# Kernel tuning notes

Measured on AMD Instinct MI355X. Metric: run time of the kernel, lower is better.

## Reference

```python
import jax, jax.numpy as jnp
import numpy as np

N_HEAD, N_MIX, D_MODEL, D_K, D_V = 8, 2, 512, 64, 64
BN_EPS = 1e-5


def avg_pool_3x3_s2(x):
    # AvgPool2d(kernel=3, stride=2, pad=1, count_include_pad=False) on NCHW
    win = (1, 1, 3, 3)
    stride = (1, 1, 2, 2)
    pad = [(0, 0), (0, 0), (1, 1), (1, 1)]
    s = jax.lax.reduce_window(x, 0.0, jax.lax.add, win, stride, pad)
    ones = jnp.ones((1, 1, x.shape[2], x.shape[3]), x.dtype)
    cnt = jax.lax.reduce_window(ones, 0.0, jax.lax.add, win, stride, pad)
    return s / cnt


def conv1x1(x, w, b=None):
    # w: [out_c, in_c]; x: [B, in_c, H, W]
    y = jnp.einsum('oc,bchw->bohw', w, x)
    if b is not None:
        y = y + b[None, :, None, None]
    return y


def setup_inputs() -> dict:
    key = jax.random.key(0)
    ks = jax.random.split(key, 8)
    B, H, W = 2, 56, 56
    std_kq = np.sqrt(2.0 / (D_MODEL + D_K)).astype(np.float32)
    std_v = np.sqrt(2.0 / (D_MODEL + D_V)).astype(np.float32)
    std_mix = np.power(N_MIX, -0.5).astype(np.float32)
    return {
        'x': jax.random.normal(ks[0], (B, D_MODEL, H, W), jnp.float32),
        'w_qs': jax.random.normal(ks[1], (N_HEAD * D_K, D_MODEL), jnp.float32) * std_kq,
        'b_qs': jnp.zeros((N_HEAD * D_K,), jnp.float32),
        'w_vs': jax.random.normal(ks[2], (N_HEAD * D_V, D_MODEL), jnp.float32) * std_v,
        'b_vs': jnp.zeros((N_HEAD * D_V,), jnp.float32),
        'mix_w': jax.random.uniform(ks[3], (N_MIX, D_K), jnp.float32, -std_mix, std_mix),
        'w_out': jax.random.normal(ks[4], (D_MODEL, N_HEAD * D_V), jnp.float32) * 0.02,
        'bn_gamma': jnp.ones((D_MODEL,), jnp.float32),
        'bn_beta': jnp.zeros((D_MODEL,), jnp.float32),
    }


def reference(x, w_qs, b_qs, w_vs, b_vs, mix_w, w_out, bn_gamma, bn_beta):
    B, C, H, W = x.shape
    N = H * W
    m = N_MIX
    d = D_K // m  # per-mixture dim
    temperature = D_K ** 0.5

    px = avg_pool_3x3_s2(x)  # [B, C, H/2, W/2]
    N2 = px.shape[2] * px.shape[3]

    # conv_ks aliases conv_qs in the original (shared weights)
    qt = conv1x1(x, w_qs, b_qs).reshape(B * N_HEAD, D_K, N)
    kt = conv1x1(px, w_qs, b_qs).reshape(B * N_HEAD, D_K, N2)
    vt = conv1x1(px, w_vs, b_vs).reshape(B * N_HEAD, D_V, N2)

    # mixture weights pi: softmax over mixtures of weight @ mean_q
    bar_qt = qt.mean(axis=2)  # [B', D_K]
    pi = jax.nn.softmax(jnp.einsum('md,bd->bm', mix_w, bar_qt), axis=1)  # [B', m]

    q = qt.reshape(B * N_HEAD * m, d, N).transpose(0, 2, 1)  # [B'm, N, d]
    k2 = kt.reshape(B * N_HEAD * m, d, N2)  # [B'm, d, N2]

    attn = jnp.einsum('bnd,bdk->bnk', q, k2) / temperature  # [B'm, N, N2]
    attn = jax.nn.softmax(attn, axis=2)
    # dropout is identity in eval mode
    attn = (attn * pi.reshape(-1, 1, 1)).reshape(B * N_HEAD, m, N, N2).sum(1)

    out = jnp.einsum('bnk,bvk->bnv', attn, vt)  # [B', N, D_V]
    out = out.transpose(0, 2, 1).reshape(B, N_HEAD * D_V, H, W)
    out = conv1x1(out, w_out)  # no bias
    # BatchNorm2d in eval mode: running_mean=0, running_var=1
    inv = 1.0 / jnp.sqrt(jnp.float32(1.0 + BN_EPS))
    out = out * inv * bn_gamma[None, :, None, None] + bn_beta[None, :, None, None]
    return out + x
```

## Files before the change

kernel.cpp:

```cpp
#include <hip/hip_runtime.h>
#include <math.h>

typedef unsigned short u16;
typedef short bf16x8 __attribute__((ext_vector_type(8)));
typedef short bf16x4 __attribute__((ext_vector_type(4)));
typedef float f32x4 __attribute__((ext_vector_type(4)));

#define MFMA(a, b, c) __builtin_amdgcn_mfma_f32_16x16x32_bf16(a, b, c, 0, 0, 0)

#define SCALE_K 0.18033688011112043f

__device__ __forceinline__ float bf2f(u16 v) {
    union { float f; unsigned u; } x;
    x.u = ((unsigned)v) << 16;
    return x.f;
}
__device__ __forceinline__ u16 f2bf(float f) {
    union { float f; unsigned u; } x;
    x.f = f;
    unsigned r = x.u + 0x7FFF + ((x.u >> 16) & 1);
    return (u16)(r >> 16);
}
__device__ __forceinline__ bf16x4 pk4(float a, float b, float c, float d) {
    union { unsigned u[2]; bf16x4 v; } x;
    asm("v_cvt_pk_bf16_f32 %0, %1, %2" : "=v"(x.u[0]) : "v"(a), "v"(b));
    asm("v_cvt_pk_bf16_f32 %0, %1, %2" : "=v"(x.u[1]) : "v"(c), "v"(d));
    return x.v;
}

__global__ __launch_bounds__(256) void cvt_kernel(const float* __restrict__ s0,
                                                  const float* __restrict__ s1,
                                                  const float* __restrict__ s2,
                                                  u16* __restrict__ d0, u16* __restrict__ d1,
                                                  u16* __restrict__ d2) {
    int i = blockIdx.x * 256 + threadIdx.x;
    const float* s = (blockIdx.y == 0) ? s0 : ((blockIdx.y == 1) ? s1 : s2);
    u16* d = (blockIdx.y == 0) ? d0 : ((blockIdx.y == 1) ? d1 : d2);
    d[i] = f2bf(s[i]);
}

__global__ __launch_bounds__(256) void transpose_kernel(const float* __restrict__ x,
                                                        u16* __restrict__ xT) {
    __shared__ u16 tile[64][65];
    int b = blockIdx.z;
    int n0 = blockIdx.x * 64, c0 = blockIdx.y * 64;
    int j = threadIdx.x & 63, q = threadIdx.x >> 6;
    const float* xb = x + b * 512 * 3136;
#pragma unroll
    for (int it = 0; it < 16; ++it) {
        int r = q * 16 + it;
        tile[r][j] = f2bf(xb[(c0 + r) * 3136 + n0 + j]);
    }
    __syncthreads();
    u16* xTb = xT + b * 3136 * 512;
#pragma unroll
    for (int it = 0; it < 16; ++it) {
        int r = q * 16 + it;
        xTb[(n0 + r) * 512 + c0 + j] = tile[j][r];
    }
}

__global__ __launch_bounds__(256) void pool_kernel(const u16* __restrict__ xT,
                                                   u16* __restrict__ pxT) {
    int n2 = blockIdx.x;
    int b = blockIdx.y;
    int t = threadIdx.x;
    int i = n2 / 28, jj = n2 % 28;
    float s0 = 0.f, s1 = 0.f;
    int cnt = 0;
    const u16* xb = xT + b * 3136 * 512;
#pragma unroll
    for (int dr = 0; dr < 3; dr++) {
        int r = 2 * i - 1 + dr;
        if (r < 0 || r >= 56) continue;
#pragma unroll
        for (int dc = 0; dc < 3; dc++) {
            int cc = 2 * jj - 1 + dc;
            if (cc < 0 || cc >= 56) continue;
            const u16* row = xb + (r * 56 + cc) * 512;
            s0 += bf2f(row[t]);
            s1 += bf2f(row[t + 256]);
            cnt++;
        }
    }
    float invc = 1.0f / (float)cnt;
    u16* op = pxT + (b * 784 + n2) * 512;
    op[t] = f2bf(s0 * invc);
    op[t + 256] = f2bf(s1 * invc);
}

__device__ __forceinline__ void gemm_core(const u16* __restrict__ A, int lda, int M,
                                          const u16* __restrict__ BT, int ldb, int Ncol,
                                          int K, int row0, int col0, f32x4 acc[4][4]) {
    int lane = threadIdx.x & 63;
    int lr = lane & 15, lg = lane >> 4;
    int ar[4], bc[4];
#pragma unroll
    for (int i = 0; i < 4; i++) {
        int r = row0 + i * 16 + lr;
        ar[i] = (r < M) ? r : (M - 1);
    }
#pragma unroll
    for (int j = 0; j < 4; j++) {
        int cj = col0 + j * 16 + lr;
        bc[j] = (cj < Ncol) ? cj : (Ncol - 1);
    }
    for (int k = 0; k < K; k += 32) {
        int ko = k + lg * 8;
        bf16x8 af[4], bfr[4];
#pragma unroll
        for (int i = 0; i < 4; i++) af[i] = *(const bf16x8*)(A + ar[i] * lda + ko);
#pragma unroll
        for (int j = 0; j < 4; j++) bfr[j] = *(const bf16x8*)(BT + bc[j] * ldb + ko);
#pragma unroll
        for (int i = 0; i < 4; i++)
#pragma unroll
            for (int j = 0; j < 4; j++) acc[i][j] = MFMA(af[i], bfr[j], acc[i][j]);
    }
}

__global__ __launch_bounds__(256) void gemm_qk(const u16* __restrict__ xT,
                                               const u16* __restrict__ W,
                                               const float* __restrict__ bias,
                                               u16* __restrict__ out, int M, int Npad,
                                               float oscale) {
    int b = blockIdx.z;
    int w = threadIdx.x >> 6;
    int row0 = blockIdx.y * 128 + (w >> 1) * 64;
    int col0 = blockIdx.x * 128 + (w & 1) * 64;
    f32x4 acc[4][4];
#pragma unroll
    for (int i = 0; i < 4; i++)
#pragma unroll
        for (int j = 0; j < 4; j++) acc[i][j] = (f32x4){0.f, 0.f, 0.f, 0.f};
    gemm_core(xT + b * M * 512, 512, M, W, 512, 512, 512, row0, col0, acc);
    int lane = threadIdx.x & 63;
    int lr = lane & 15, lg = lane >> 4;
#pragma unroll
    for (int j = 0; j < 4; j++) {
        int oc = col0 + j * 16 + lr;
        float bs = bias[oc];
        int bh = b * 8 + (oc >> 6), dk = oc & 63;
        u16* op = out + (bh * Npad) * 64 + dk;
#pragma unroll
        for (int i = 0; i < 4; i++) {
#pragma unroll
            for (int r = 0; r < 4; r++) {
                int n = row0 + i * 16 + lg * 4 + r;
                if (n < M) op[n * 64] = f2bf((acc[i][j][r] + bs) * oscale);
                else if (n < Npad) op[n * 64] = 0;
            }
        }
    }
}

__global__ __launch_bounds__(256) void gemm_v(const u16* __restrict__ W,
                                              const u16* __restrict__ pxT,
                                              const float* __restrict__ bias,
                                              u16* __restrict__ vt) {
    int b = blockIdx.z;
    int w = threadIdx.x >> 6;
    int row0 = blockIdx.y * 128 + (w >> 1) * 64;
    int col0 = blockIdx.x * 128 + (w & 1) * 64;
    f32x4 acc[4][4];
#pragma unroll
    for (int i = 0; i < 4; i++)
#pragma unroll
        for (int j = 0; j < 4; j++) acc[i][j] = (f32x4){0.f, 0.f, 0.f, 0.f};
    gemm_core(W, 512, 512, pxT + b * 784 * 512, 512, 784, 512, row0, col0, acc);
    int lane = threadIdx.x & 63;
    int lr = lane & 15, lg = lane >> 4;
#pragma unroll
    for (int i = 0; i < 4; i++) {
#pragma unroll
        for (int r = 0; r < 4; r++) {
            int oc = row0 + i * 16 + lg * 4 + r;
            float bs = bias[oc];
            u16* vp = vt + ((b * 8 + (oc >> 6)) * 64 + (oc & 63)) * 800;
#pragma unroll
            for (int j = 0; j < 4; j++) {
                int n2 = col0 + j * 16 + lr;
                if (n2 < 784) vp[n2] = f2bf(acc[i][j][r] + bs);
                else if (n2 < 800) vp[n2] = 0;
            }
        }
    }
}

__global__ __launch_bounds__(256) void pi_stage1(const u16* __restrict__ qt,
                                                 float* __restrict__ part) {
    __shared__ float red[4][64];
    int chunk = blockIdx.x, bh = blockIdx.y;
    int t = threadIdx.x, dk = t & 63, seg = t >> 6;
    const u16* q = qt + (bh * 3136 + chunk * 112) * 64 + dk;
    float s = 0.f;
    for (int n = seg; n < 112; n += 4) s += bf2f(q[n * 64]);
    red[seg][dk] = s;
    __syncthreads();
    if (t < 64) part[(bh * 28 + chunk) * 64 + t] =
        red[0][t] + red[1][t] + red[2][t] + red[3][t];
}

__global__ __launch_bounds__(64) void pi_stage2(const float* __restrict__ part,
                                                const float* __restrict__ mix_w,
                                                float* __restrict__ pi) {
    int bh = blockIdx.x, lane = threadIdx.x;
    float bar = 0.f;
#pragma unroll
    for (int c = 0; c < 28; c++) bar += part[(bh * 28 + c) * 64 + lane];
    bar *= (1.0f / 3136.0f);
    float l0 = mix_w[lane] * bar;
    float l1 = mix_w[64 + lane] * bar;
#pragma unroll
    for (int d = 1; d < 64; d <<= 1) {
        l0 += __shfl_xor(l0, d);
        l1 += __shfl_xor(l1, d);
    }
    if (lane == 0) {
        float mx = fmaxf(l0, l1);
        float e0 = __expf(l0 - mx), e1 = __expf(l1 - mx);
        float inv = 1.0f / (e0 + e1);
        pi[bh * 2 + 0] = e0 * inv;
        pi[bh * 2 + 1] = e1 * inv;
    }
}

__global__ __launch_bounds__(256) void attn_kernel(const u16* __restrict__ qt,
                                                   const u16* __restrict__ kt,
                                                   const u16* __restrict__ vt,
                                                   const float* __restrict__ pi,
                                                   u16* __restrict__ ao) {
    int w = threadIdx.x >> 6, lane = threadIdx.x & 63;
    int lr = lane & 15, lg = lane >> 4;
    int bh = blockIdx.x & 15;
    int xq = blockIdx.x >> 4;
    int qbase = (xq * 4 + w) * 16;
    const u16* qp = qt + (bh * 3136 + qbase) * 64;
    const u16* kp = kt + bh * 800 * 64;
    const u16* vp = vt + bh * 64 * 800;

    bf16x8 qf[2];
    qf[0] = *(const bf16x8*)(qp + lr * 64 + lg * 8);
    qf[1] = *(const bf16x8*)(qp + lr * 64 + 32 + lg * 8);

    f32x4 O[2][4];
    float lsum[2] = {0.f, 0.f};
#pragma unroll
    for (int m = 0; m < 2; m++)
#pragma unroll
        for (int t = 0; t < 4; t++) O[m][t] = (f32x4){0.f, 0.f, 0.f, 0.f};

    auto loadK = [&](int base, bf16x8 (*kf)[2]) {
#pragma unroll
        for (int m = 0; m < 2; m++) {
            kf[m][0] = *(const bf16x8*)(kp + (base + lr) * 64 + m * 32 + lg * 8);
            kf[m][1] = *(const bf16x8*)(kp + (base + 16 + lr) * 64 + m * 32 + lg * 8);
        }
    };
    auto loadV = [&](int base, bf16x4* v0, bf16x4* v1) {
#pragma unroll
        for (int t = 0; t < 4; t++) {
            v0[t] = *(const bf16x4*)(vp + (t * 16 + lr) * 800 + base + lg * 4);
            v1[t] = *(const bf16x4*)(vp + (t * 16 + lr) * 800 + base + 16 + lg * 4);
        }
    };
    auto compute = [&](bf16x8 (*kf)[2], bf16x4* v0, bf16x4* v1, bool tail) {
#pragma unroll
        for (int m = 0; m < 2; m++) {
            f32x4 s0 = MFMA(kf[m][0], qf[m], ((f32x4){0.f, 0.f, 0.f, 0.f}));
            f32x4 s1 = MFMA(kf[m][1], qf[m], ((f32x4){0.f, 0.f, 0.f, 0.f}));
            float p0 = __builtin_amdgcn_exp2f(s0[0]);
            float p1 = __builtin_amdgcn_exp2f(s0[1]);
            float p2 = __builtin_amdgcn_exp2f(s0[2]);
            float p3 = __builtin_amdgcn_exp2f(s0[3]);
            float p4 = __builtin_amdgcn_exp2f(s1[0]);
            float p5 = __builtin_amdgcn_exp2f(s1[1]);
            float p6 = __builtin_amdgcn_exp2f(s1[2]);
            float p7 = __builtin_amdgcn_exp2f(s1[3]);
            if (tail) { p4 = 0.f; p5 = 0.f; p6 = 0.f; p7 = 0.f; }
            lsum[m] += ((p0 + p1) + (p2 + p3)) + ((p4 + p5) + (p6 + p7));
            union { bf16x4 h[2]; bf16x8 w8; } pa;
            pa.h[0] = pk4(p0, p1, p2, p3);
            pa.h[1] = pk4(p4, p5, p6, p7);
#pragma unroll
            for (int t = 0; t < 4; t++) {
                union { bf16x4 h[2]; bf16x8 w8; } vv;
                vv.h[0] = v0[t];
                vv.h[1] = v1[t];
                O[m][t] = MFMA(pa.w8, vv.w8, O[m][t]);
            }
        }
    };

    bf16x8 kfA[2][2], kfB[2][2];
    bf16x4 v0A[4], v1A[4], v0B[4], v1B[4];
    loadK(0, kfA);
    loadV(0, v0A, v1A);
    for (int c = 0; c < 24; c += 2) {
        loadK((c + 1) * 32, kfB);
        loadV((c + 1) * 32, v0B, v1B);
        compute(kfA, v0A, v1A, false);
        loadK((c + 2) * 32, kfA);
        loadV((c + 2) * 32, v0A, v1A);
        compute(kfB, v0B, v1B, false);
    }
    compute(kfA, v0A, v1A, true);

#pragma unroll
    for (int m = 0; m < 2; m++) {
        lsum[m] += __shfl_xor(lsum[m], 16);
        lsum[m] += __shfl_xor(lsum[m], 32);
    }
    float pi0 = pi[bh * 2], pi1 = pi[bh * 2 + 1];
    int b = bh >> 3, h = bh & 7;
    u16* aop = ao + ((b * 3136 + qbase) * 512) + h * 64;
#pragma unroll
    for (int t = 0; t < 4; t++) {
#pragma unroll
        for (int r = 0; r < 4; r++) {
            int n = lg * 4 + r;
            float l0 = __shfl(lsum[0], n);
            float l1 = __shfl(lsum[1], n);
            float v = (pi0 / l0) * O[0][t][r] + (pi1 / l1) * O[1][t][r];
            aop[n * 512 + t * 16 + lr] = f2bf(v);
        }
    }
}

__global__ __launch_bounds__(256) void gemm_out(const u16* __restrict__ W,
                                                const u16* __restrict__ aoT,
                                                const float* __restrict__ gamma,
                                                const float* __restrict__ beta,
                                                const float* __restrict__ xres,
                                                float* __restrict__ out) {
    int b = blockIdx.z;
    int w = threadIdx.x >> 6;
    int row0 = blockIdx.y * 128 + (w >> 1) * 64;
    int col0 = blockIdx.x * 128 + (w & 1) * 64;
    f32x4 acc[4][4];
#pragma unroll
    for (int i = 0; i < 4; i++)
#pragma unroll
        for (int j = 0; j < 4; j++) acc[i][j] = (f32x4){0.f, 0.f, 0.f, 0.f};
    gemm_core(W, 512, 512, aoT + b * 3136 * 512, 512, 3136, 512, row0, col0, acc);
    const float inv = 0.99999500003749969f;
    int lane = threadIdx.x & 63;
    int lr = lane & 15, lg = lane >> 4;
#pragma unroll
    for (int i = 0; i < 4; i++) {
#pragma unroll
        for (int r = 0; r < 4; r++) {
            int oc = row0 + i * 16 + lg * 4 + r;
            float g = gamma[oc] * inv;
            float bt = beta[oc];
            const float* xp = xres + (b * 512 + oc) * 3136;
            float* op = out + (b * 512 + oc) * 3136;
#pragma unroll
            for (int j = 0; j < 4; j++) {
                int n = col0 + j * 16 + lr;
                if (n < 3136) op[n] = acc[i][j][r] * g + bt + xp[n];
            }
        }
    }
}

extern "C" void kernel_launch(void* const* d_in, const int* in_sizes, int n_in,
                              void* d_out, int out_size, void* d_ws, size_t ws_size,
                              hipStream_t stream) {
    const float* x = (const float*)d_in[0];
    const float* w_qs = (const float*)d_in[1];
    const float* b_qs = (const float*)d_in[2];
    const float* w_vs = (const float*)d_in[3];
    const float* b_vs = (const float*)d_in[4];
    const float* mix_w = (const float*)d_in[5];
    const float* w_out = (const float*)d_in[6];
    const float* gamma = (const float*)d_in[7];
    const float* beta = (const float*)d_in[8];
    float* out = (float*)d_out;

    char* ws = (char*)d_ws;
    u16* xT = (u16*)(ws + 0);
    u16* ao = (u16*)(ws + 0);
    u16* pxT = (u16*)(ws + 6422528);
    u16* qt = (u16*)(ws + 8028160);
    u16* kt = (u16*)(ws + 14450688);
    u16* vt = (u16*)(ws + 16089088);
    u16* wq_b = (u16*)(ws + 17727488);
    u16* wv_b = (u16*)(ws + 18251776);
    u16* wo_b = (u16*)(ws + 18776064);
    float* pi = (float*)(ws + 19300352);
    float* part = (float*)(ws + 19300480);

    hipLaunchKernelGGL(cvt_kernel, dim3(1024, 3), dim3(256), 0, stream, w_qs, w_vs, w_out,
                       wq_b, wv_b, wo_b);
    hipLaunchKernelGGL(transpose_kernel, dim3(49, 8, 2), dim3(256), 0, stream, x, xT);
    hipLaunchKernelGGL(pool_kernel, dim3(784, 2), dim3(256), 0, stream, xT, pxT);
    hipLaunchKernelGGL(gemm_qk, dim3(4, 25, 2), dim3(256), 0, stream, xT, wq_b, b_qs, qt,
                       3136, 3136, 1.0f);
    hipLaunchKernelGGL(gemm_qk, dim3(4, 7, 2), dim3(256), 0, stream, pxT, wq_b, b_qs, kt,
                       784, 800, SCALE_K);
    hipLaunchKernelGGL(gemm_v, dim3(7, 4, 2), dim3(256), 0, stream, wv_b, pxT, b_vs, vt);
    hipLaunchKernelGGL(pi_stage1, dim3(28, 16), dim3(256), 0, stream, qt, part);
    hipLaunchKernelGGL(pi_stage2, dim3(16), dim3(64), 0, stream, part, mix_w, pi);
    hipLaunchKernelGGL(attn_kernel, dim3(784), dim3(256), 0, stream, qt, kt, vt, pi, ao);
    hipLaunchKernelGGL(gemm_out, dim3(25, 4, 2), dim3(256), 0, stream, wo_b, ao, gamma,
                       beta, x, out);
}
```

Baseline: 242.7 us.

## Split attention KV range across waves with LDS reduction of partial outputs

Each block now handles a single 16-query tile, and its four waves each process a disjoint slice of the 25 key chunks, where previously each wave swept all keys for its own query tile. Partial output accumulators and row sums are written to shared memory and reduced across waves before normalisation and the bf16 store. The grid grows fourfold to expose more parallelism and shorten each wave's serial chain. In exchange it drops the explicit double-buffered prefetch, reloads Q per block, and adds LDS traffic and a barrier.

Result: faster. 229.1 us (-5.6%).

```diff
diff --git a/kernel.cpp b/kernel.cpp
--- a/kernel.cpp
+++ b/kernel.cpp
@@ -230,100 +230,119 @@
                                                    const u16* __restrict__ vt,
                                                    const float* __restrict__ pi,
                                                    u16* __restrict__ ao) {
+    __shared__ float ldsO[8][16][65];
+    __shared__ float ldsL[8][16];
     int w = threadIdx.x >> 6, lane = threadIdx.x & 63;
     int lr = lane & 15, lg = lane >> 4;
     int bh = blockIdx.x & 15;
-    int xq = blockIdx.x >> 4;
-    int qbase = (xq * 4 + w) * 16;
+    int qti = blockIdx.x >> 4;
+    int qbase = qti * 16;
     const u16* qp = qt + (bh * 3136 + qbase) * 64;
-    const u16* kp = kt + bh * 800 * 64;
-    const u16* vp = vt + bh * 64 * 800;
-
-    bf16x8 qf[2];
-    qf[0] = *(const bf16x8*)(qp + lr * 64 + lg * 8);
-    qf[1] = *(const bf16x8*)(qp + lr * 64 + 32 + lg * 8);
-
-    f32x4 O[2][4];
-    float lsum[2] = {0.f, 0.f};
-#pragma unroll
-    for (int m = 0; m < 2; m++)
-#pragma unroll
-        for (int t = 0; t < 4; t++) O[m][t] = (f32x4){0.f, 0.f, 0.f, 0.f};
-
-    auto loadK = [&](int base, bf16x8 (*kf)[2]) {
-#pragma unroll
-        for (int m = 0; m < 2; m++) {
-            kf[m][0] = *(const bf16x8*)(kp + (base + lr) * 64 + m * 32 + lg * 8);
-            kf[m][1] = *(const bf16x8*)(kp + (base + 16 + lr) * 64 + m * 32 + lg * 8);
-        }
-    };
-    auto loadV = [&](int base, bf16x4* v0, bf16x4* v1) {
-#pragma unroll
-        for (int t = 0; t < 4; t++) {
-            v0[t] = *(const bf16x4*)(vp + (t * 16 + lr) * 800 + base + lg * 4);
-            v1[t] = *(const bf16x4*)(vp + (t * 16 + lr) * 800 + base + 16 + lg * 4);
-        }
-    };
-    auto compute = [&](bf16x8 (*kf)[2], bf16x4* v0, bf16x4* v1, bool tail) {
-#pragma unroll
-        for (int m = 0; m < 2; m++) {
-            f32x4 s0 = MFMA(kf[m][0], qf[m], ((f32x4){0.f, 0.f, 0.f, 0.f}));
-            f32x4 s1 = MFMA(kf[m][1], qf[m], ((f32x4){0.f, 0.f, 0.f, 0.f}));
-            float p0 = __builtin_amdgcn_exp2f(s0[0]);
-            float p1 = __builtin_amdgcn_exp2f(s0[1]);
-            float p2 = __builtin_amdgcn_exp2f(s0[2]);
-            float p3 = __builtin_amdgcn_exp2f(s0[3]);
-            float p4 = __builtin_amdgcn_exp2f(s1[0]);
-            float p5 = __builtin_amdgcn_exp2f(s1[1]);
-            float p6 = __builtin_amdgcn_exp2f(s1[2]);
-            float p7 = __builtin_amdgcn_exp2f(s1[3]);
-            if (tail) { p4 = 0.f; p5 = 0.f; p6 = 0.f; p7 = 0.f; }
-            lsum[m] += ((p0 + p1) + (p2 + p3)) + ((p4 + p5) + (p6 + p7));
-            union { bf16x4 h[2]; bf16x8 w8; } pa;
-            pa.h[0] = pk4(p0, p1, p2, p3);
-            pa.h[1] = pk4(p4, p5, p6, p7);
-#pragma unroll
-            for (int t = 0; t < 4; t++) {
-                union { bf16x4 h[2]; bf16x8 w8; } vv;
-                vv.h[0] = v0[t];
-                vv.h[1] = v1[t];
-                O[m][t] = MFMA(pa.w8, vv.w8, O[m][t]);
-            }
-        }
-    };
-
-    bf16x8 kfA[2][2], kfB[2][2];
-    bf16x4 v0A[4], v1A[4], v0B[4], v1B[4];
-    loadK(0, kfA);
-    loadV(0, v0A, v1A);
-    for (int c = 0; c < 24; c += 2) {
-        loadK((c + 1) * 32, kfB);
-        loadV((c + 1) * 32, v0B, v1B);
-        compute(kfA, v0A, v1A, false);
-        loadK((c + 2) * 32, kfA);
-        loadV((c + 2) * 32, v0A, v1A);
-        compute(kfB, v0B, v1B, false);
-    }
-    compute(kfA, v0A, v1A, true);
-
-#pragma unroll
-    for (int m = 0; m < 2; m++) {
-        lsum[m] += __shfl_xor(lsum[m], 16);
-        lsum[m] += __shfl_xor(lsum[m], 32);
-    }
+    const u16* kbase = kt + bh * 800 * 64 + lr * 64 + lg * 8;
+    const u16* vbase = vt + bh * 64 * 800 + lr * 800 + lg * 4;
+
+    bf16x8 qf0 = *(const bf16x8*)(qp + lr * 64 + lg * 8);
+    bf16x8 qf1 = *(const bf16x8*)(qp + lr * 64 + 32 + lg * 8);
+
+    const f32x4 z4 = {0.f, 0.f, 0.f, 0.f};
+    f32x4 O00 = z4, O01 = z4, O02 = z4, O03 = z4;
+    f32x4 O10 = z4, O11 = z4, O12 = z4, O13 = z4;
+    float ls0 = 0.f, ls1 = 0.f;
+
+    int start = (w == 0) ? 0 : 1 + 6 * w;
+    int end = start + ((w == 0) ? 7 : 6);
+    for (int c = start; c < end; ++c) {
+        int base = c * 32;
+        bool tail = (c == 24);
+        bf16x8 k00 = *(const bf16x8*)(kbase + base * 64);
+        bf16x8 k01 = *(const bf16x8*)(kbase + (base + 16) * 64);
+        bf16x8 k10 = *(const bf16x8*)(kbase + base * 64 + 32);
+        bf16x8 k11 = *(const bf16x8*)(kbase + (base + 16) * 64 + 32);
+        bf16x4 va0 = *(const bf16x4*)(vbase + base);
+        bf16x4 va1 = *(const bf16x4*)(vbase + base + 16 * 800);
+        bf16x4 va2 = *(const bf16x4*)(vbase + base + 32 * 800);
+        bf16x4 va3 = *(const bf16x4*)(vbase + base + 48 * 800);
+        bf16x4 vb0 = *(const bf16x4*)(vbase + base + 16);
+        bf16x4 vb1 = *(const bf16x4*)(vbase + base + 16 + 16 * 800);
+        bf16x4 vb2 = *(const bf16x4*)(vbase + base + 16 + 32 * 800);
+        bf16x4 vb3 = *(const bf16x4*)(vbase + base + 16 + 48 * 800);
+        union { bf16x4 h[2]; bf16x8 w8; } vv0, vv1, vv2, vv3, pa;
+        vv0.h[0] = va0; vv0.h[1] = vb0;
+        vv1.h[0] = va1; vv1.h[1] = vb1;
+        vv2.h[0] = va2; vv2.h[1] = vb2;
+        vv3.h[0] = va3; vv3.h[1] = vb3;
+        f32x4 s0 = MFMA(k00, qf0, z4);
+        f32x4 s1 = MFMA(k01, qf0, z4);
+        float p0 = __builtin_amdgcn_exp2f(s0[0]);
+        float p1 = __builtin_amdgcn_exp2f(s0[1]);
+        float p2 = __builtin_amdgcn_exp2f(s0[2]);
+        float p3 = __builtin_amdgcn_exp2f(s0[3]);
+        float p4 = __builtin_amdgcn_exp2f(s1[0]);
+        float p5 = __builtin_amdgcn_exp2f(s1[1]);
+        float p6 = __builtin_amdgcn_exp2f(s1[2]);
+        float p7 = __builtin_amdgcn_exp2f(s1[3]);
+        if (tail) { p4 = 0.f; p5 = 0.f; p6 = 0.f; p7 = 0.f; }
+        ls0 += ((p0 + p1) + (p2 + p3)) + ((p4 + p5) + (p6 + p7));
+        pa.h[0] = pk4(p0, p1, p2, p3);
+        pa.h[1] = pk4(p4, p5, p6, p7);
+        O00 = MFMA(pa.w8, vv0.w8, O00);
+        O01 = MFMA(pa.w8, vv1.w8, O01);
+        O02 = MFMA(pa.w8, vv2.w8, O02);
+        O03 = MFMA(pa.w8, vv3.w8, O03);
+        s0 = MFMA(k10, qf1, z4);
+        s1 = MFMA(k11, qf1, z4);
+        p0 = __builtin_amdgcn_exp2f(s0[0]);
+        p1 = __builtin_amdgcn_exp2f(s0[1]);
+        p2 = __builtin_amdgcn_exp2f(s0[2]);
+        p3 = __builtin_amdgcn_exp2f(s0[3]);
+        p4 = __builtin_amdgcn_exp2f(s1[0]);
+        p5 = __builtin_amdgcn_exp2f(s1[1]);
+        p6 = __builtin_amdgcn_exp2f(s1[2]);
+        p7 = __builtin_amdgcn_exp2f(s1[3]);
+        if (tail) { p4 = 0.f; p5 = 0.f; p6 = 0.f; p7 = 0.f; }
+        ls1 += ((p0 + p1) + (p2 + p3)) + ((p4 + p5) + (p6 + p7));
+        pa.h[0] = pk4(p0, p1, p2, p3);
+        pa.h[1] = pk4(p4, p5, p6, p7);
+        O10 = MFMA(pa.w8, vv0.w8, O10);
+        O11 = MFMA(pa.w8, vv1.w8, O11);
+        O12 = MFMA(pa.w8, vv2.w8, O12);
+        O13 = MFMA(pa.w8, vv3.w8, O13);
+    }
+
+    ls0 += __shfl_xor(ls0, 16);
+    ls0 += __shfl_xor(ls0, 32);
+    ls1 += __shfl_xor(ls1, 16);
+    ls1 += __shfl_xor(ls1, 32);
+    if (lane < 16) {
+        ldsL[w * 2 + 0][lr] = ls0;
+        ldsL[w * 2 + 1][lr] = ls1;
+    }
+#define PUTO(T, OA, OB)                              \
+    {                                                \
+        _Pragma("unroll") for (int r = 0; r < 4; r++) { \
+            ldsO[w * 2 + 0][lg * 4 + r][(T)*16 + lr] = OA[r]; \
+            ldsO[w * 2 + 1][lg * 4 + r][(T)*16 + lr] = OB[r]; \
+        }                                            \
+    }
+    PUTO(0, O00, O10)
+    PUTO(1, O01, O11)
+    PUTO(2, O02, O12)
+    PUTO(3, O03, O13)
+#undef PUTO
+    __syncthreads();
+
     float pi0 = pi[bh * 2], pi1 = pi[bh * 2 + 1];
+    int col = threadIdx.x & 63, rg = threadIdx.x >> 6;
     int b = bh >> 3, h = bh & 7;
     u16* aop = ao + ((b * 3136 + qbase) * 512) + h * 64;
 #pragma unroll
-    for (int t = 0; t < 4; t++) {
-#pragma unroll
-        for (int r = 0; r < 4; r++) {
-            int n = lg * 4 + r;
-            float l0 = __shfl(lsum[0], n);
-            float l1 = __shfl(lsum[1], n);
-            float v = (pi0 / l0) * O[0][t][r] + (pi1 / l1) * O[1][t][r];
-            aop[n * 512 + t * 16 + lr] = f2bf(v);
-        }
+    for (int i = 0; i < 4; i++) {
+        int q = rg * 4 + i;
+        float l0 = ldsL[0][q] + ldsL[2][q] + ldsL[4][q] + ldsL[6][q];
+        float l1 = ldsL[1][q] + ldsL[3][q] + ldsL[5][q] + ldsL[7][q];
+        float o0 = ldsO[0][q][col] + ldsO[2][q][col] + ldsO[4][q][col] + ldsO[6][q][col];
+        float o1 = ldsO[1][q][col] + ldsO[3][q][col] + ldsO[5][q][col] + ldsO[7][q][col];
+        aop[q * 512 + col] = f2bf((pi0 / l0) * o0 + (pi1 / l1) * o1);
     }
 }
 
@@ -402,7 +421,7 @@
     hipLaunchKernelGGL(gemm_v, dim3(7, 4, 2), dim3(256), 0, stream, wv_b, pxT, b_vs, vt);
     hipLaunchKernelGGL(pi_stage1, dim3(28, 16), dim3(256), 0, stream, qt, part);
     hipLaunchKernelGGL(pi_stage2, dim3(16), dim3(64), 0, stream, part, mix_w, pi);
-    hipLaunchKernelGGL(attn_kernel, dim3(784), dim3(256), 0, stream, qt, kt, vt, pi, ao);
+    hipLaunchKernelGGL(attn_kernel, dim3(3136), dim3(256), 0, stream, qt, kt, vt, pi, ao);
     hipLaunchKernelGGL(gemm_out, dim3(25, 4, 2), dim3(256), 0, stream, wo_b, ao, gamma,
                        beta, x, out);
 }
```
